# Kernel optimization log

Hardware: AMD Instinct MI355X
Metric: run time of the kernel (lower is better)

## Reference

```python
import jax, jax.numpy as jnp
import numpy as np


def setup_inputs() -> dict:
    key = jax.random.key(0)
    kz, kx = jax.random.split(key, 2)
    N, C, k, m = 16, 256, 8, 63
    z = jax.random.uniform(kz, (N, C, k, k), dtype=jnp.float32)
    x = jax.random.uniform(kx, (N, C, m, m), dtype=jnp.float32)
    weights = jnp.ones((1, C, 1, 1, 1), dtype=jnp.float32)
    return {"z": z, "x": x, "weights": weights}


def reference(z, x, weights):
    # Bhattacharyya coefficient between template z (N,C,k,k) and every kxk
    # sliding window of x (N,C,m,m):
    #   out[n,0,i,j] = (1/k^2) * sum_{c,p,q} w[c] * sqrt(x[n,c,i+p,j+q] * z[n,c,p,q])
    # Since inputs are nonnegative, sqrt(x*z) == sqrt(x)*sqrt(z), so the whole
    # unfold + sqrt-multiply + channel-sum + spatial-mean collapses into a
    # per-sample VALID cross-correlation of sqrt(x) with w*sqrt(z) -- no im2col
    # tensor is ever materialized.
    N, C, k, _ = z.shape
    m = x.shape[2]
    mo = m - k + 1
    w = weights.reshape(1, C, 1, 1)          # per-channel weight
    lhs = jnp.sqrt(x).reshape(1, N * C, m, m)  # fold batch into channel groups
    rhs = w * jnp.sqrt(z)                     # (N, C, k, k) per-sample kernels
    out = jax.lax.conv_general_dilated(
        lhs, rhs,
        window_strides=(1, 1), padding="VALID",
        feature_group_count=N,                # group n uses sample n's kernel
        dimension_numbers=("NCHW", "OIHW", "NCHW"))  # (1, N, mo, mo)
    return out.reshape(N, 1, mo, mo) / (k * k)
```

## Files before the change

kernel.cpp:

```cpp
#include <hip/hip_runtime.h>
#include <math.h>


#define NS 16
#define NC 256
#define MI 63
#define MO 56
#define NPIX (MI*MI)
#define NOUT (MO*MO)

#define IH 8
#define NBAND 7
#define CSPLIT 8
#define NCH (NC/CSPLIT)
#define G 8
#define NG (NCH/G)
#define XROWS (IH+7)
#define XW (XROWS*MI)
#define XCP 948
#define ZROW 72
#define UPITCH 66

typedef __attribute__((ext_vector_type(8))) short bf16x8;
typedef __attribute__((ext_vector_type(4))) float f32x4;
typedef __attribute__((address_space(3))) unsigned lds_u32;
typedef const __attribute__((address_space(1))) unsigned glb_u32;

static __device__ __forceinline__ short f2bf(float f) {
    union { float f; unsigned u; } v; v.f = f;
    return (short)((v.u + 0x7fffu + ((v.u >> 16) & 1u)) >> 16);
}

__global__ __launch_bounds__(512, 2)
void bhat_u(const float* __restrict__ z, const float* __restrict__ x,
            const float* __restrict__ w, float* __restrict__ out) {
    __shared__ float xs[2 * G * XCP];
    __shared__ short zf[NG * 8 * ZROW];
    float* U = xs;

    const int n    = blockIdx.x;
    const int band = blockIdx.y;
    const int c0   = blockIdx.z * NCH;
    const int tid  = threadIdx.x;
    const int i0   = band * IH;
    const int wave = tid >> 6, lane = tid & 63;

    auto stage = [&](int g, int buf) {
        const float* src = x + (size_t)(n * NC + c0 + g * G + wave) * NPIX + (size_t)i0 * MI;
        float* dst = &xs[buf * (G * XCP) + wave * XCP];
        #pragma unroll
        for (int it = 0; it < XW / 64; ++it)
            __builtin_amdgcn_global_load_lds((glb_u32*)(src + it * 64 + lane),
                                             (lds_u32*)(dst + it * 64), 4, 0, 0);
        if (lane < XW - (XW / 64) * 64)
            __builtin_amdgcn_global_load_lds((glb_u32*)(src + (XW / 64) * 64 + lane),
                                             (lds_u32*)(dst + (XW / 64) * 64), 4, 0, 0);
    };

    stage(0, 0);

    {
        const float* zb = z + ((size_t)n * NC + c0) * 64;
        for (int idx = tid; idx < NG * 8 * 64; idx += 512) {
            int g = idx >> 9, rem = idx & 511;
            int q = rem >> 6, k = rem & 63;
            int cl = (k & 31) >> 2;
            int p  = ((k >> 5) << 2) + (k & 3);
            float v = w[c0 + g * G + cl] *
                      __builtin_amdgcn_sqrtf(zb[(size_t)(g * G + cl) * 64 + p * 8 + q]);
            zf[(g * 8 + q) * ZROW + k] = f2bf(v);
        }
    }

    asm volatile("s_waitcnt vmcnt(0)" ::: "memory");
    __syncthreads();

    const int wj = wave & 3, wh = wave >> 2;
    const int lm = lane & 15, lg = lane >> 4;
    const int jb = wj * 16;
    const int rb = wh * 4;

    f32x4 acc[4];
    #pragma unroll
    for (int il = 0; il < 4; ++il) acc[il] = (f32x4){0.f, 0.f, 0.f, 0.f};

    for (int g = 0; g < NG; ++g) {
        if (g + 1 < NG) stage(g + 1, (g + 1) & 1);

        const float* xb = &xs[(g & 1) * (G * XCP)];
        float xr[2][11];
        #pragma unroll
        for (int ci = 0; ci < 2; ++ci)
            #pragma unroll
            for (int r = 0; r < 11; ++r)
                xr[ci][r] = __builtin_amdgcn_sqrtf(
                    xb[(lg * 2 + ci) * XCP + (rb + r) * MI + jb + lm]);

        bf16x8 af[2];
        #pragma unroll
        for (int ks = 0; ks < 2; ++ks)
            af[ks] = *(const bf16x8*)(&zf[(g * 8 + (lm & 7)) * ZROW + ks * 32 + lg * 8]);

        #pragma unroll
        for (int il = 0; il < 4; ++il) {
            #pragma unroll
            for (int ks = 0; ks < 2; ++ks) {
                const int b = il + ks * 4;
                union { bf16x8 v; unsigned u[4]; } bf;
                asm("v_cvt_pk_bf16_f32 %0, %1, %2" : "=v"(bf.u[0]) : "v"(xr[0][b]),   "v"(xr[0][b+1]));
                asm("v_cvt_pk_bf16_f32 %0, %1, %2" : "=v"(bf.u[1]) : "v"(xr[0][b+2]), "v"(xr[0][b+3]));
                asm("v_cvt_pk_bf16_f32 %0, %1, %2" : "=v"(bf.u[2]) : "v"(xr[1][b]),   "v"(xr[1][b+1]));
                asm("v_cvt_pk_bf16_f32 %0, %1, %2" : "=v"(bf.u[3]) : "v"(xr[1][b+2]), "v"(xr[1][b+3]));
                acc[il] = __builtin_amdgcn_mfma_f32_16x16x32_bf16(af[ks], bf.v, acc[il], 0, 0, 0);
            }
        }
        asm volatile("s_waitcnt vmcnt(0)" ::: "memory");
        __syncthreads();
    }

    if (lg < 2) {
        #pragma unroll
        for (int il = 0; il < 4; ++il) {
            const int iloc = rb + il;
            #pragma unroll
            for (int t = 0; t < 4; ++t)
                U[(iloc * 8 + lg * 4 + t) * UPITCH + jb + lm] = acc[il][t];
        }
    }
    __syncthreads();

    if (tid < IH * MO) {
        const int il = tid / MO, j = tid - il * MO;
        float s = 0.f;
        #pragma unroll
        for (int q = 0; q < 8; ++q)
            s += U[(il * 8 + q) * UPITCH + j + q];
        atomicAdd(&out[(size_t)n * NOUT + (size_t)(i0 + il) * MO + j], s * (1.0f / 64.0f));
    }
}

extern "C" void kernel_launch(void* const* d_in, const int* in_sizes, int n_in,
                              void* d_out, int out_size, void* d_ws, size_t ws_size,
                              hipStream_t stream) {
    const float* z = (const float*)d_in[0];
    const float* x = (const float*)d_in[1];
    const float* w = (const float*)d_in[2];
    float* out = (float*)d_out;

    hipMemsetAsync(out, 0, (size_t)out_size * sizeof(float), stream);

    dim3 grid(NS, NBAND, CSPLIT);
    bhat_u<<<grid, 512, 0, stream>>>(z, x, w, out);
}
```

Baseline: 106.8 us.

## Halve channel split, double-buffer template weights per group, raise occupancy hint

```diff
diff --git a/kernel.cpp b/kernel.cpp
--- a/kernel.cpp
+++ b/kernel.cpp
@@ -11,7 +11,7 @@
 
 #define IH 8
 #define NBAND 7
-#define CSPLIT 8
+#define CSPLIT 4
 #define NCH (NC/CSPLIT)
 #define G 8
 #define NG (NCH/G)
@@ -31,11 +31,11 @@
     return (short)((v.u + 0x7fffu + ((v.u >> 16) & 1u)) >> 16);
 }
 
-__global__ __launch_bounds__(512, 2)
+__global__ __launch_bounds__(512, 4)
 void bhat_u(const float* __restrict__ z, const float* __restrict__ x,
             const float* __restrict__ w, float* __restrict__ out) {
     __shared__ float xs[2 * G * XCP];
-    __shared__ short zf[NG * 8 * ZROW];
+    __shared__ short zf[2 * 8 * ZROW];
     float* U = xs;
 
     const int n    = blockIdx.x;
@@ -44,6 +44,14 @@
     const int tid  = threadIdx.x;
     const int i0   = band * IH;
     const int wave = tid >> 6, lane = tid & 63;
+
+    const int zq = tid >> 6, zk = tid & 63;
+    const int zcl = (zk & 31) >> 2;
+    const int zp  = ((zk >> 5) << 2) + (zk & 3);
+    const float* zptr = z + ((size_t)n * NC + c0 + zcl) * 64 + zp * 8 + zq;
+    float wv[NG];
+    #pragma unroll
+    for (int g = 0; g < NG; ++g) wv[g] = w[c0 + g * G + zcl];
 
     auto stage = [&](int g, int buf) {
         const float* src = x + (size_t)(n * NC + c0 + g * G + wave) * NPIX + (size_t)i0 * MI;
@@ -58,20 +66,10 @@
     };
 
     stage(0, 0);
-
     {
-        const float* zb = z + ((size_t)n * NC + c0) * 64;
-        for (int idx = tid; idx < NG * 8 * 64; idx += 512) {
-            int g = idx >> 9, rem = idx & 511;
-            int q = rem >> 6, k = rem & 63;
-            int cl = (k & 31) >> 2;
-            int p  = ((k >> 5) << 2) + (k & 3);
-            float v = w[c0 + g * G + cl] *
-                      __builtin_amdgcn_sqrtf(zb[(size_t)(g * G + cl) * 64 + p * 8 + q]);
-            zf[(g * 8 + q) * ZROW + k] = f2bf(v);
-        }
+        float zv = *zptr;
+        zf[zq * ZROW + zk] = f2bf(wv[0] * __builtin_amdgcn_sqrtf(zv));
     }
-
     asm volatile("s_waitcnt vmcnt(0)" ::: "memory");
     __syncthreads();
 
@@ -84,8 +82,13 @@
     #pragma unroll
     for (int il = 0; il < 4; ++il) acc[il] = (f32x4){0.f, 0.f, 0.f, 0.f};
 
+    #pragma unroll
     for (int g = 0; g < NG; ++g) {
-        if (g + 1 < NG) stage(g + 1, (g + 1) & 1);
+        float znext = 0.f;
+        if (g + 1 < NG) {
+            stage(g + 1, (g + 1) & 1);
+            znext = zptr[(g + 1) * G * 64];
+        }
 
         const float* xb = &xs[(g & 1) * (G * XCP)];
         float xr[2][11];
@@ -99,7 +102,7 @@
         bf16x8 af[2];
         #pragma unroll
         for (int ks = 0; ks < 2; ++ks)
-            af[ks] = *(const bf16x8*)(&zf[(g * 8 + (lm & 7)) * ZROW + ks * 32 + lg * 8]);
+            af[ks] = *(const bf16x8*)(&zf[(g & 1) * 8 * ZROW + (lm & 7) * ZROW + ks * 32 + lg * 8]);
 
         #pragma unroll
         for (int il = 0; il < 4; ++il) {
@@ -114,6 +117,11 @@
                 acc[il] = __builtin_amdgcn_mfma_f32_16x16x32_bf16(af[ks], bf.v, acc[il], 0, 0, 0);
             }
         }
+
+        if (g + 1 < NG)
+            zf[((g + 1) & 1) * 8 * ZROW + zq * ZROW + zk] =
+                f2bf(wv[g + 1] * __builtin_amdgcn_sqrtf(znext));
+
         asm volatile("s_waitcnt vmcnt(0)" ::: "memory");
         __syncthreads();
     }
```

After: 103.3 us. 3.2% less time.
